# Performance work log

Measured on AMD Instinct MI355X. Metric: run time of the kernel, lower is better.

The kernel has to match this reference:

```python
import jax, jax.numpy as jnp
import numpy as np

N, E = 50000, 800000
IN, HID, H, OUT = 128, 32, 4, 32
NEG_SLOPE = 0.2


def _gatv2_layer(x, edge_index, Wl, bl, Wr, br, att, bias, heads, ch, concat):
    """One GATv2Conv layer (PyG semantics: add self-loops, lin_l on source,
    lin_r on target, e = att . leaky_relu(gl_src + gr_dst), segment softmax
    over incoming edges of each target, scatter-add weighted source messages)."""
    n = x.shape[0]
    loop = jnp.arange(n)
    src = jnp.concatenate([edge_index[0], loop])
    dst = jnp.concatenate([edge_index[1], loop])

    gl = (x @ Wl + bl).reshape(n, heads, ch)   # source transform [N,H,C]
    gr = (x @ Wr + br).reshape(n, heads, ch)   # target transform [N,H,C]

    m = jax.nn.leaky_relu(gl[src] + gr[dst], NEG_SLOPE)   # [E+N,H,C]
    e = jnp.einsum('ehc,hc->eh', m, att)                   # [E+N,H]

    # numerically stable segment softmax over dst
    emax = jax.lax.stop_gradient(jax.ops.segment_max(e, dst, num_segments=n))
    ex = jnp.exp(e - emax[dst])
    denom = jax.ops.segment_sum(ex, dst, num_segments=n)
    alpha = ex / denom[dst]                                # [E+N,H]

    out = jax.ops.segment_sum(alpha[:, :, None] * gl[src], dst, num_segments=n)  # [N,H,C]
    out = out.reshape(n, heads * ch) if concat else out.mean(axis=1)
    return out + bias


def setup_inputs() -> dict:
    key = jax.random.key(0)
    ks = jax.random.split(key, 16)
    s = 0.05
    return {
        'x': jax.random.normal(ks[0], (N, IN), dtype=jnp.float32),
        'edge_index': jax.random.randint(ks[1], (2, E), 0, N, dtype=jnp.int32),
        # layer 1: IN -> HID, H heads, concat
        'Wl1': jax.random.normal(ks[2], (IN, H * HID), dtype=jnp.float32) * s,
        'bl1': jnp.zeros((H * HID,), dtype=jnp.float32),
        'Wr1': jax.random.normal(ks[3], (IN, H * HID), dtype=jnp.float32) * s,
        'br1': jnp.zeros((H * HID,), dtype=jnp.float32),
        'att1': jax.random.normal(ks[4], (H, HID), dtype=jnp.float32) * s,
        'bias1': jnp.zeros((H * HID,), dtype=jnp.float32),
        # layer 2: H*HID -> OUT, 1 head, no concat
        'Wl2': jax.random.normal(ks[5], (H * HID, OUT), dtype=jnp.float32) * s,
        'bl2': jnp.zeros((OUT,), dtype=jnp.float32),
        'Wr2': jax.random.normal(ks[6], (H * HID, OUT), dtype=jnp.float32) * s,
        'br2': jnp.zeros((OUT,), dtype=jnp.float32),
        'att2': jax.random.normal(ks[7], (1, OUT), dtype=jnp.float32) * s,
        'bias2': jnp.zeros((OUT,), dtype=jnp.float32),
    }


def reference(x, edge_index, Wl1, bl1, Wr1, br1, att1, bias1,
              Wl2, bl2, Wr2, br2, att2, bias2):
    h = jax.nn.elu(_gatv2_layer(x, edge_index, Wl1, bl1, Wr1, br1, att1, bias1, H, HID, True))
    # dropout inactive in eval mode
    return _gatv2_layer(h, edge_index, Wl2, bl2, Wr2, br2, att2, bias2, 1, OUT, False)
```

## Files before the change

kernel.cpp:

```cpp
#include <hip/hip_runtime.h>

#define NNODES 50000
#define NEDGES 800000
#define ETOT   (NNODES + NEDGES)
#define NEG 0.2f
#define BKTS 196
#define P1E 4096
#define NP1 ((ETOT + P1E - 1) / P1E)
#define GEMM1_NB ((NNODES + 31) / 32)
#define GEMM1_H1 782
#define GEMM1_H2 (GEMM1_NB - GEMM1_H1)

typedef unsigned short ushort_t;
typedef unsigned int uint_t;
typedef __attribute__((ext_vector_type(8))) short short8;
typedef __attribute__((ext_vector_type(4))) float f32x4;

__device__ __forceinline__ ushort_t f2bf(float f) {
  uint_t u = __float_as_uint(f);
  u += 0x7FFFu + ((u >> 16) & 1u);
  return (ushort_t)(u >> 16);
}
__device__ __forceinline__ float bf2f(ushort_t h) {
  return __uint_as_float((uint_t)h << 16);
}


__device__ __forceinline__ void coarse_hist_body(int bid, int tid,
    const int* __restrict__ ei, int* __restrict__ pcnt, int* c ) {
  for (int i = tid; i < BKTS; i += 256) c[i] = 0;
  __syncthreads();
  int e0 = bid * P1E;
#pragma unroll
  for (int t = 0; t < P1E / 256; ++t) {
    int i = e0 + t * 256 + tid;
    if (i < ETOT) {
      int dst = (i < NEDGES) ? ei[NEDGES + i] : (i - NEDGES);
      atomicAdd(&c[dst >> 8], 1);
    }
  }
  __syncthreads();
  for (int i = tid; i < BKTS; i += 256)
    pcnt[i * NP1 + bid] = c[i];
}

__device__ __forceinline__ void prep_w_body(int k, int n,
    const float* __restrict__ Wl1, const float* __restrict__ Wr1,
    ushort_t* __restrict__ WtHi, ushort_t* __restrict__ WtLo) {
  float w = (n < 128) ? Wl1[k * 128 + n] : Wr1[k * 128 + (n - 128)];
  ushort_t h = f2bf(w);
  WtHi[n * 128 + k] = h;
  WtLo[n * 128 + k] = f2bf(w - bf2f(h));
}

__device__ __forceinline__ void bin1_body(int bid, int tid,
    const int* __restrict__ ei, const int* __restrict__ bucketStart,
    const int* __restrict__ goffArr, uint_t* __restrict__ binned, char* smemc) {
  int* cnt   = (int*)smemc;
  int* pref  = cnt + BKTS;
  int* fillL = pref + BKTS;
  uint_t* stage = (uint_t*)(fillL + BKTS);
  int e0 = bid * P1E;
  for (int i = tid; i < BKTS; i += 256) { cnt[i] = 0; fillL[i] = 0; }
  __syncthreads();
  uint_t mypk[P1E / 256];
#pragma unroll
  for (int t = 0; t < P1E / 256; ++t) {
    int i = e0 + t * 256 + tid;
    if (i < ETOT) {
      int dst = (i < NEDGES) ? ei[NEDGES + i] : (i - NEDGES);
      int src = (i < NEDGES) ? ei[i] : dst;
      int b = dst >> 8;
      mypk[t] = (uint_t)src | ((uint_t)(dst & 255) << 16) | ((uint_t)b << 24);
      atomicAdd(&cnt[b], 1);
    } else mypk[t] = 0xFFFFFFFFu;
  }
  __syncthreads();
  if (tid < 64) {
    int carry = 0;
    for (int k0 = 0; k0 < BKTS; k0 += 64) {
      int k = k0 + tid;
      int v = (k < BKTS) ? cnt[k] : 0;
      int s = v;
      for (int off = 1; off < 64; off <<= 1) {
        int u = __shfl_up(s, off);
        if (tid >= off) s += u;
      }
      if (k < BKTS) pref[k] = carry + s - v;
      carry += __shfl(s, 63);
    }
  }
  __syncthreads();
#pragma unroll
  for (int t = 0; t < P1E / 256; ++t) {
    uint_t pk = mypk[t];
    int b = pk >> 24;
    if (b < BKTS) {
      int p = pref[b] + atomicAdd(&fillL[b], 1);
      stage[p] = pk;
    }
  }
  __syncthreads();
  int total = (e0 + P1E <= ETOT) ? P1E : (ETOT - e0);
  for (int j = tid; j < total; j += 256) {
    uint_t pk = stage[j];
    int b = pk >> 24;
    binned[bucketStart[b] + goffArr[b * NP1 + bid] + (j - pref[b])] = pk;
  }
}

__device__ __forceinline__ void bin2_body(int b, int tid,
    const uint_t* __restrict__ binned, const int* __restrict__ bucketStart,
    int* __restrict__ rowptr, int* __restrict__ csrc, char* smemc) {
  int* cnt   = (int*)smemc;
  int* pref  = cnt + 256;
  int* fillL = pref + 256;
  int* outS  = fillL + 256;
  int base = bucketStart[b];
  int cntAll = bucketStart[b + 1] - base;
  cnt[tid] = 0; fillL[tid] = 0;
  __syncthreads();
  for (int j = tid; j < cntAll; j += 256)
    atomicAdd(&cnt[(binned[base + j] >> 16) & 255], 1);
  __syncthreads();
  if (tid < 64) {
    int carry = 0;
    for (int k0 = 0; k0 < 256; k0 += 64) {
      int k = k0 + tid;
      int v = cnt[k];
      int s = v;
      for (int off = 1; off < 64; off <<= 1) {
        int u = __shfl_up(s, off);
        if (tid >= off) s += u;
      }
      pref[k] = carry + s - v;
      carry += __shfl(s, 63);
    }
  }
  __syncthreads();
  int node = b * 256 + tid;
  if (node < NNODES) rowptr[node] = base + pref[tid];
  for (int j = tid; j < cntAll; j += 256) {
    uint_t pk = binned[base + j];
    int d = (pk >> 16) & 255;
    int p = pref[d] + atomicAdd(&fillL[d], 1);
    outS[p] = (int)(pk & 0xFFFF);
  }
  __syncthreads();
  for (int j = tid; j < cntAll; j += 256)
    csrc[base + j] = outS[j];
}

__device__ __forceinline__ void gemm1_body(int m0, int tid,
    const float* __restrict__ x,
    const ushort_t* __restrict__ WtHi, const ushort_t* __restrict__ WtLo,
    const float* __restrict__ bl1, const float* __restrict__ br1,
    ushort_t* __restrict__ gl1, ushort_t* __restrict__ gr1, char* smem) {
  constexpr int LDA = 132;
  ushort_t (*Ahi)[LDA] = (ushort_t(*)[LDA])smem;
  ushort_t (*Alo)[LDA] = (ushort_t(*)[LDA])(smem + 32 * LDA * 2);
  float (*Cs)[260] = (float(*)[260])smem;
#pragma unroll
  for (int i = 0; i < 4; ++i) {
    int it = i * 256 + tid;
    int row = it >> 5, c4 = it & 31;
    int gm = m0 + row;
    float4 v = (gm < NNODES) ? *(const float4*)&x[(size_t)gm * 128 + 4 * c4]
                             : make_float4(0.f, 0.f, 0.f, 0.f);
    ushort_t h0 = f2bf(v.x), h1 = f2bf(v.y), h2 = f2bf(v.z), h3 = f2bf(v.w);
    ushort_t l0 = f2bf(v.x - bf2f(h0)), l1 = f2bf(v.y - bf2f(h1));
    ushort_t l2 = f2bf(v.z - bf2f(h2)), l3 = f2bf(v.w - bf2f(h3));
    uint2 ph, pl;
    ph.x = (uint_t)h0 | ((uint_t)h1 << 16); ph.y = (uint_t)h2 | ((uint_t)h3 << 16);
    pl.x = (uint_t)l0 | ((uint_t)l1 << 16); pl.y = (uint_t)l2 | ((uint_t)l3 << 16);
    *(uint2*)&Ahi[row][4 * c4] = ph;
    *(uint2*)&Alo[row][4 * c4] = pl;
  }
  __syncthreads();
  int wave = tid >> 6, lane = tid & 63;
  int quad = lane >> 4, nl = lane & 15;
  int nb = wave * 64;
  f32x4 acc[2][4];
#pragma unroll
  for (int tm = 0; tm < 2; ++tm)
#pragma unroll
    for (int tn = 0; tn < 4; ++tn) acc[tm][tn] = (f32x4){0.f, 0.f, 0.f, 0.f};

#pragma unroll
  for (int kc = 0; kc < 4; ++kc) {
    int klane = kc * 32 + quad * 8;
    short8 ah[2], al[2], bh[4], bl[4];
#pragma unroll
    for (int tm = 0; tm < 2; ++tm) {
      ah[tm] = *(const short8*)&Ahi[16 * tm + nl][klane];
      al[tm] = *(const short8*)&Alo[16 * tm + nl][klane];
    }
#pragma unroll
    for (int tn = 0; tn < 4; ++tn) {
      size_t wo = (size_t)(nb + 16 * tn + nl) * 128 + klane;
      bh[tn] = *(const short8*)&WtHi[wo];
      bl[tn] = *(const short8*)&WtLo[wo];
    }
#pragma unroll
    for (int tm = 0; tm < 2; ++tm)
#pragma unroll
      for (int tn = 0; tn < 4; ++tn) {
        acc[tm][tn] = __builtin_amdgcn_mfma_f32_16x16x32_bf16(ah[tm], bh[tn], acc[tm][tn], 0, 0, 0);
        acc[tm][tn] = __builtin_amdgcn_mfma_f32_16x16x32_bf16(ah[tm], bl[tn], acc[tm][tn], 0, 0, 0);
        acc[tm][tn] = __builtin_amdgcn_mfma_f32_16x16x32_bf16(al[tm], bh[tn], acc[tm][tn], 0, 0, 0);
      }
  }
  float bb[4];
#pragma unroll
  for (int tn = 0; tn < 4; ++tn) {
    int n = nb + 16 * tn + nl;
    bb[tn] = (n < 128) ? bl1[n] : br1[n - 128];
  }
  __syncthreads();
#pragma unroll
  for (int tm = 0; tm < 2; ++tm)
#pragma unroll
    for (int tn = 0; tn < 4; ++tn)
#pragma unroll
      for (int r = 0; r < 4; ++r)
        Cs[16 * tm + 4 * quad + r][nb + 16 * tn + nl] = acc[tm][tn][r] + bb[tn];
  __syncthreads();
#pragma unroll
  for (int i = 0; i < 2; ++i) {
    int it = i * 256 + tid;
    int row = it >> 4, oc = (it & 15) * 8;
    int gm = m0 + row;
    if (gm < NNODES) {
      uint4 pk;
      pk.x = (uint_t)f2bf(Cs[row][oc + 0]) | ((uint_t)f2bf(Cs[row][oc + 1]) << 16);
      pk.y = (uint_t)f2bf(Cs[row][oc + 2]) | ((uint_t)f2bf(Cs[row][oc + 3]) << 16);
      pk.z = (uint_t)f2bf(Cs[row][oc + 4]) | ((uint_t)f2bf(Cs[row][oc + 5]) << 16);
      pk.w = (uint_t)f2bf(Cs[row][oc + 6]) | ((uint_t)f2bf(Cs[row][oc + 7]) << 16);
      *(uint4*)&gl1[(size_t)gm * 128 + oc] = pk;
    }
  }
#pragma unroll
  for (int i = 0; i < 2; ++i) {
    int it = i * 256 + tid;
    int row = it >> 4, oc = (it & 15) * 8;
    int gm = m0 + row;
    if (gm < NNODES) {
      uint4 pk;
      pk.x = (uint_t)f2bf(Cs[row][128 + oc + 0]) | ((uint_t)f2bf(Cs[row][128 + oc + 1]) << 16);
      pk.y = (uint_t)f2bf(Cs[row][128 + oc + 2]) | ((uint_t)f2bf(Cs[row][128 + oc + 3]) << 16);
      pk.z = (uint_t)f2bf(Cs[row][128 + oc + 4]) | ((uint_t)f2bf(Cs[row][128 + oc + 5]) << 16);
      pk.w = (uint_t)f2bf(Cs[row][128 + oc + 6]) | ((uint_t)f2bf(Cs[row][128 + oc + 7]) << 16);
      *(uint4*)&gr1[(size_t)gm * 128 + oc] = pk;
    }
  }
}


__global__ __launch_bounds__(256) void fusedA(const int* __restrict__ ei,
    int* __restrict__ pcnt,
    const float* __restrict__ Wl1, const float* __restrict__ Wr1,
    ushort_t* __restrict__ WtHi, ushort_t* __restrict__ WtLo) {
  __shared__ int c[BKTS];
  int bid = blockIdx.x, tid = threadIdx.x;
  if (bid < NP1) coarse_hist_body(bid, tid, ei, pcnt, c);
  else           prep_w_body(bid - NP1, tid, Wl1, Wr1, WtHi, WtLo);
}

__global__ __launch_bounds__(64) void coarse_scan(const int* __restrict__ pcnt,
                                                  int* __restrict__ goffArr,
                                                  int* __restrict__ tot) {
  int b = blockIdx.x;
  int lane = threadIdx.x;
  int carry = 0;
  for (int k0 = 0; k0 < NP1; k0 += 64) {
    int k = k0 + lane;
    int v = (k < NP1) ? pcnt[b * NP1 + k] : 0;
    int s = v;
    for (int off = 1; off < 64; off <<= 1) {
      int u = __shfl_up(s, off);
      if (lane >= off) s += u;
    }
    if (k < NP1) goffArr[b * NP1 + k] = carry + s - v;
    carry += __shfl(s, 63);
  }
  if (lane == 0) tot[b] = carry;
}

__global__ __launch_bounds__(64) void bucket_scan(const int* __restrict__ tot,
                                                  int* __restrict__ bucketStart,
                                                  int* __restrict__ rowptr) {
  int lane = threadIdx.x;
  int carry = 0;
  for (int k0 = 0; k0 < BKTS; k0 += 64) {
    int k = k0 + lane;
    int v = (k < BKTS) ? tot[k] : 0;
    int s = v;
    for (int off = 1; off < 64; off <<= 1) {
      int u = __shfl_up(s, off);
      if (lane >= off) s += u;
    }
    if (k < BKTS) bucketStart[k] = carry + s - v;
    carry += __shfl(s, 63);
  }
  if (lane == 0) {
    bucketStart[BKTS] = carry;
    rowptr[NNODES] = ETOT;
  }
}

__global__ __launch_bounds__(256) void fusedB(const int* __restrict__ ei,
    const int* __restrict__ bucketStart, const int* __restrict__ goffArr,
    uint_t* __restrict__ binned,
    const float* __restrict__ x,
    const ushort_t* __restrict__ WtHi, const ushort_t* __restrict__ WtLo,
    const float* __restrict__ bl1, const float* __restrict__ br1,
    ushort_t* __restrict__ gl1, ushort_t* __restrict__ gr1) {
  __shared__ __align__(16) char smem[32 * 260 * 4];
  int bid = blockIdx.x, tid = threadIdx.x;
  if (bid < NP1) bin1_body(bid, tid, ei, bucketStart, goffArr, binned, smem);
  else gemm1_body((bid - NP1) * 32, tid, x, WtHi, WtLo, bl1, br1, gl1, gr1, smem);
}

__global__ __launch_bounds__(256) void fusedC(const uint_t* __restrict__ binned,
    const int* __restrict__ bucketStart, int* __restrict__ rowptr,
    int* __restrict__ csrc,
    const float* __restrict__ x,
    const ushort_t* __restrict__ WtHi, const ushort_t* __restrict__ WtLo,
    const float* __restrict__ bl1, const float* __restrict__ br1,
    ushort_t* __restrict__ gl1, ushort_t* __restrict__ gr1) {
  __shared__ __align__(16) char smem[32 * 260 * 4];
  int bid = blockIdx.x, tid = threadIdx.x;
  if (bid < BKTS) bin2_body(bid, tid, binned, bucketStart, rowptr, csrc, smem);
  else gemm1_body((GEMM1_H1 + bid - BKTS) * 32, tid, x, WtHi, WtLo, bl1, br1, gl1, gr1, smem);
}

__global__ __launch_bounds__(128) void gemm2_tile(
    const ushort_t* __restrict__ A,
    const float* __restrict__ W1, const float* __restrict__ b1,
    const float* __restrict__ W2, const float* __restrict__ b2,
    ushort_t* __restrict__ G1, ushort_t* __restrict__ G2) {
  constexpr int K = 128, KC = 32, BM = 128, BN = 64, MCOLS = 32, NT = 128;
  constexpr int LDA = BM + 4;
  __shared__ float AsT[KC][LDA];
  __shared__ float Ws[KC][BN];
  int row0 = blockIdx.x * BM;
  int tid = threadIdx.x;
  int tx = tid % (BN / 8), ty = tid / (BN / 8);
  float acc[8][8];
#pragma unroll
  for (int i = 0; i < 8; ++i)
#pragma unroll
    for (int j = 0; j < 8; ++j) acc[i][j] = 0.f;

  for (int kc = 0; kc < K; kc += KC) {
#pragma unroll
    for (int item = tid; item < BM * (KC / 4); item += NT) {
      int r = item >> 3, f4 = item & 7;
      int grow = row0 + r;
      uint2 u = (grow < NNODES)
          ? *(const uint2*)&A[(size_t)grow * K + kc + 4 * f4]
          : make_uint2(0u, 0u);
      AsT[4 * f4 + 0][r] = __uint_as_float(u.x << 16);
      AsT[4 * f4 + 1][r] = __uint_as_float(u.x & 0xffff0000u);
      AsT[4 * f4 + 2][r] = __uint_as_float(u.y << 16);
      AsT[4 * f4 + 3][r] = __uint_as_float(u.y & 0xffff0000u);
    }
#pragma unroll
    for (int item = tid; item < KC * (BN / 4); item += NT) {
      int k = item / (BN / 4), c4 = item % (BN / 4);
      int ccat = 4 * c4;
      const float* src = (ccat < MCOLS)
          ? &W1[(size_t)(kc + k) * MCOLS + ccat]
          : &W2[(size_t)(kc + k) * MCOLS + ccat - MCOLS];
      *(float4*)&Ws[k][4 * c4] = *(const float4*)src;
    }
    __syncthreads();
#pragma unroll 8
    for (int k = 0; k < KC; ++k) {
      float4 a0 = *(const float4*)&AsT[k][4 * ty];
      float4 a1 = *(const float4*)&AsT[k][BM / 2 + 4 * ty];
      float4 w0 = *(const float4*)&Ws[k][4 * tx];
      float4 w1 = *(const float4*)&Ws[k][BN / 2 + 4 * tx];
      float av[8] = {a0.x, a0.y, a0.z, a0.w, a1.x, a1.y, a1.z, a1.w};
      float wv[8] = {w0.x, w0.y, w0.z, w0.w, w1.x, w1.y, w1.z, w1.w};
#pragma unroll
      for (int i = 0; i < 8; ++i)
#pragma unroll
        for (int j = 0; j < 8; ++j) acc[i][j] = fmaf(av[i], wv[j], acc[i][j]);
    }
    __syncthreads();
  }
#pragma unroll
  for (int i = 0; i < 8; ++i) {
    int row = row0 + (i < 4 ? 4 * ty + i : BM / 2 + 4 * ty + (i - 4));
    if (row >= NNODES) continue;
#pragma unroll
    for (int jj = 0; jj < 2; ++jj) {
      int ccat = (jj == 0 ? 4 * tx : BN / 2 + 4 * tx);
      float o0 = acc[i][4 * jj + 0], o1 = acc[i][4 * jj + 1];
      float o2 = acc[i][4 * jj + 2], o3 = acc[i][4 * jj + 3];
      if (ccat < MCOLS) {
        float4 bb = *(const float4*)&b1[ccat];
        uint2 pk;
        pk.x = (uint_t)f2bf(o0 + bb.x) | ((uint_t)f2bf(o1 + bb.y) << 16);
        pk.y = (uint_t)f2bf(o2 + bb.z) | ((uint_t)f2bf(o3 + bb.w) << 16);
        *(uint2*)&G1[(size_t)row * MCOLS + ccat] = pk;
      } else {
        int c = ccat - MCOLS;
        float4 bb = *(const float4*)&b2[c];
        uint2 pk;
        pk.x = (uint_t)f2bf(o0 + bb.x) | ((uint_t)f2bf(o1 + bb.y) << 16);
        pk.y = (uint_t)f2bf(o2 + bb.z) | ((uint_t)f2bf(o3 + bb.w) << 16);
        *(uint2*)&G2[(size_t)row * MCOLS + c] = pk;
      }
    }
  }
}

__global__ __launch_bounds__(128) void gat1_edge(const int* __restrict__ rowptr,
                          const int* __restrict__ csrc,
                          const ushort_t* __restrict__ glb,
                          const ushort_t* __restrict__ grb,
                          const float* __restrict__ att, const float* __restrict__ bias,
                          ushort_t* __restrict__ hout) {
  int node = blockIdx.x * 2 + (threadIdx.x >> 6);
  if (node >= NNODES) return;
  int lane = threadIdx.x & 63;
  int eslot = lane >> 4;
  int q = lane & 15;
  int c8 = q * 8;
  const float C6 = 0.8656170245333781f;
  const float C4 = 0.5770780163555854f;
  float4 av0 = *(const float4*)(att + c8);
  float4 av1 = *(const float4*)(att + c8 + 4);
  float4 a60, a61, a40, a41;
  a60.x = C6 * av0.x; a60.y = C6 * av0.y; a60.z = C6 * av0.z; a60.w = C6 * av0.w;
  a61.x = C6 * av1.x; a61.y = C6 * av1.y; a61.z = C6 * av1.z; a61.w = C6 * av1.w;
  a40.x = C4 * av0.x; a40.y = C4 * av0.y; a40.z = C4 * av0.z; a40.w = C4 * av0.w;
  a41.x = C4 * av1.x; a41.y = C4 * av1.y; a41.z = C4 * av1.z; a41.w = C4 * av1.w;
  uint4 ug = *(const uint4*)(grb + (size_t)node * 128 + c8);
  float4 gr0, gr1v;
  gr0.x = __uint_as_float(ug.x << 16);  gr0.y = __uint_as_float(ug.x & 0xffff0000u);
  gr0.z = __uint_as_float(ug.y << 16);  gr0.w = __uint_as_float(ug.y & 0xffff0000u);
  gr1v.x = __uint_as_float(ug.z << 16); gr1v.y = __uint_as_float(ug.z & 0xffff0000u);
  gr1v.z = __uint_as_float(ug.w << 16); gr1v.w = __uint_as_float(ug.w & 0xffff0000u);
  int start = rowptr[node], end = rowptr[node + 1];
  float denom = 0.f;
  float4 A0 = make_float4(0.f, 0.f, 0.f, 0.f);
  float4 A1 = make_float4(0.f, 0.f, 0.f, 0.f);
  const char* glc = (const char*)glb;
  uint_t coff = (uint_t)(c8 * 2);
  for (int b = start; b < end; b += 64) {
    int nb = end - b; if (nb > 64) nb = 64;
    int sidx = (lane < nb) ? csrc[b + lane] : 0;
    bool pv0 = eslot < nb;
    int s0 = __shfl(sidx, eslot);
    uint4 up0 = *(const uint4*)(glc + (((uint_t)s0 << 8) + coff));
    int j1 = 4 + eslot;
    bool pv1 = j1 < nb;
    int s1 = __shfl(sidx, pv1 ? j1 : 0);
    uint4 up1 = *(const uint4*)(glc + (((uint_t)s1 << 8) + coff));
    for (int j = 0; j < nb; j += 4) {
      int jn = j + 8 + eslot;
      bool pvn = jn < nb;
      int sn = __shfl(sidx, pvn ? jn : 0);
      uint4 upn = *(const uint4*)(glc + (((uint_t)sn << 8) + coff));
      float4 g0, g1;
      g0.x = __uint_as_float(up0.x << 16);
      g0.y = __uint_as_float(up0.x & 0xffff0000u);
      g0.z = __uint_as_float(up0.y << 16);
      g0.w = __uint_as_float(up0.y & 0xffff0000u);
      g1.x = __uint_as_float(up0.z << 16);
      g1.y = __uint_as_float(up0.z & 0xffff0000u);
      g1.z = __uint_as_float(up0.w << 16);
      g1.w = __uint_as_float(up0.w & 0xffff0000u);
      float t, v;
      t = g0.x + gr0.x;  v = fmaf(a40.x, fabsf(t), a60.x * t);
      t = g0.y + gr0.y;  v = fmaf(a60.y, t, v); v = fmaf(a40.y, fabsf(t), v);
      t = g0.z + gr0.z;  v = fmaf(a60.z, t, v); v = fmaf(a40.z, fabsf(t), v);
      t = g0.w + gr0.w;  v = fmaf(a60.w, t, v); v = fmaf(a40.w, fabsf(t), v);
      t = g1.x + gr1v.x; v = fmaf(a61.x, t, v); v = fmaf(a41.x, fabsf(t), v);
      t = g1.y + gr1v.y; v = fmaf(a61.y, t, v); v = fmaf(a41.y, fabsf(t), v);
      t = g1.z + gr1v.z; v = fmaf(a61.z, t, v); v = fmaf(a41.z, fabsf(t), v);
      t = g1.w + gr1v.w; v = fmaf(a61.w, t, v); v = fmaf(a41.w, fabsf(t), v);
      v += __shfl_xor(v, 1); v += __shfl_xor(v, 2);
      float ex = pv0 ? exp2f(v) : 0.f;
      denom += ex;
      A0.x = fmaf(ex, g0.x, A0.x); A0.y = fmaf(ex, g0.y, A0.y);
      A0.z = fmaf(ex, g0.z, A0.z); A0.w = fmaf(ex, g0.w, A0.w);
      A1.x = fmaf(ex, g1.x, A1.x); A1.y = fmaf(ex, g1.y, A1.y);
      A1.z = fmaf(ex, g1.z, A1.z); A1.w = fmaf(ex, g1.w, A1.w);
      up0 = up1; pv0 = pv1;
      up1 = upn; pv1 = pvn;
    }
  }
  denom += __shfl_xor(denom, 16); denom += __shfl_xor(denom, 32);
  A0.x += __shfl_xor(A0.x, 16); A0.x += __shfl_xor(A0.x, 32);
  A0.y += __shfl_xor(A0.y, 16); A0.y += __shfl_xor(A0.y, 32);
  A0.z += __shfl_xor(A0.z, 16); A0.z += __shfl_xor(A0.z, 32);
  A0.w += __shfl_xor(A0.w, 16); A0.w += __shfl_xor(A0.w, 32);
  A1.x += __shfl_xor(A1.x, 16); A1.x += __shfl_xor(A1.x, 32);
  A1.y += __shfl_xor(A1.y, 16); A1.y += __shfl_xor(A1.y, 32);
  A1.z += __shfl_xor(A1.z, 16); A1.z += __shfl_xor(A1.z, 32);
  A1.w += __shfl_xor(A1.w, 16); A1.w += __shfl_xor(A1.w, 32);
  if (eslot < 2) {
    float inv = __builtin_amdgcn_rcpf(denom);
    float4 Ax;
    Ax.x = (eslot == 0) ? A0.x : A1.x;
    Ax.y = (eslot == 0) ? A0.y : A1.y;
    Ax.z = (eslot == 0) ? A0.z : A1.z;
    Ax.w = (eslot == 0) ? A0.w : A1.w;
    int off = c8 + 4 * eslot;
    float4 bv = *(const float4*)(bias + off);
    float o0 = Ax.x * inv + bv.x, o1 = Ax.y * inv + bv.y;
    float o2 = Ax.z * inv + bv.z, o3 = Ax.w * inv + bv.w;
    o0 = o0 > 0.f ? o0 : __expf(o0) - 1.f;
    o1 = o1 > 0.f ? o1 : __expf(o1) - 1.f;
    o2 = o2 > 0.f ? o2 : __expf(o2) - 1.f;
    o3 = o3 > 0.f ? o3 : __expf(o3) - 1.f;
    uint2 pk;
    pk.x = (uint_t)f2bf(o0) | ((uint_t)f2bf(o1) << 16);
    pk.y = (uint_t)f2bf(o2) | ((uint_t)f2bf(o3) << 16);
    *(uint2*)&hout[(size_t)node * 128 + off] = pk;
  }
}

__global__ __launch_bounds__(128) void gat2_edge(const int* __restrict__ rowptr,
                          const int* __restrict__ csrc,
                          const ushort_t* __restrict__ gl, const ushort_t* __restrict__ gr,
                          const float* __restrict__ att, const float* __restrict__ bias,
                          float* __restrict__ out) {
  int node = blockIdx.x * 2 + (threadIdx.x >> 6);
  if (node >= NNODES) return;
  int lane = threadIdx.x & 63;
  int eslot = lane >> 3;
  int q = lane & 7;
  int c4 = q * 4;
  const float C6 = 0.8656170245333781f;
  const float C4f = 0.5770780163555854f;
  float4 avc = *(const float4*)(att + c4);
  float4 a6, a4;
  a6.x = C6 * avc.x; a6.y = C6 * avc.y; a6.z = C6 * avc.z; a6.w = C6 * avc.w;
  a4.x = C4f * avc.x; a4.y = C4f * avc.y; a4.z = C4f * avc.z; a4.w = C4f * avc.w;
  uint2 ugr = *(const uint2*)(gr + (size_t)node * 32 + c4);
  float4 grd;
  grd.x = __uint_as_float(ugr.x << 16); grd.y = __uint_as_float(ugr.x & 0xffff0000u);
  grd.z = __uint_as_float(ugr.y << 16); grd.w = __uint_as_float(ugr.y & 0xffff0000u);
  int start = rowptr[node], end = rowptr[node + 1];
  float denom = 0.f;
  float4 A = make_float4(0.f, 0.f, 0.f, 0.f);
  const char* glc = (const char*)gl;
  uint_t coff = (uint_t)(c4 * 2);
  for (int b = start; b < end; b += 64) {
    int nb = end - b; if (nb > 64) nb = 64;
    int sidx = (lane < nb) ? csrc[b + lane] : 0;
    bool pv0 = eslot < nb;
    int s0 = __shfl(sidx, eslot);
    uint2 u0 = *(const uint2*)(glc + (((uint_t)s0 << 6) + coff));
    int j1 = 8 + eslot;
    bool pv1 = j1 < nb;
    int s1 = __shfl(sidx, pv1 ? j1 : 0);
    uint2 u1 = *(const uint2*)(glc + (((uint_t)s1 << 6) + coff));
    for (int j = 0; j < nb; j += 8) {
      int jn = j + 16 + eslot;
      bool pvn = jn < nb;
      int sn = __shfl(sidx, pvn ? jn : 0);
      uint2 un = *(const uint2*)(glc + (((uint_t)sn << 6) + coff));
      float4 g;
      g.x = __uint_as_float(u0.x << 16); g.y = __uint_as_float(u0.x & 0xffff0000u);
      g.z = __uint_as_float(u0.y << 16); g.w = __uint_as_float(u0.y & 0xffff0000u);
      float t, v;
      t = g.x + grd.x; v = fmaf(a4.x, fabsf(t), a6.x * t);
      t = g.y + grd.y; v = fmaf(a6.y, t, v); v = fmaf(a4.y, fabsf(t), v);
      t = g.z + grd.z; v = fmaf(a6.z, t, v); v = fmaf(a4.z, fabsf(t), v);
      t = g.w + grd.w; v = fmaf(a6.w, t, v); v = fmaf(a4.w, fabsf(t), v);
      v += __shfl_xor(v, 1); v += __shfl_xor(v, 2); v += __shfl_xor(v, 4);
      float ex = pv0 ? exp2f(v) : 0.f;
      denom += ex;
      A.x = fmaf(ex, g.x, A.x); A.y = fmaf(ex, g.y, A.y);
      A.z = fmaf(ex, g.z, A.z); A.w = fmaf(ex, g.w, A.w);
      u0 = u1; pv0 = pv1;
      u1 = un; pv1 = pvn;
    }
  }
  denom += __shfl_xor(denom, 8); denom += __shfl_xor(denom, 16); denom += __shfl_xor(denom, 32);
  A.x += __shfl_xor(A.x, 8); A.x += __shfl_xor(A.x, 16); A.x += __shfl_xor(A.x, 32);
  A.y += __shfl_xor(A.y, 8); A.y += __shfl_xor(A.y, 16); A.y += __shfl_xor(A.y, 32);
  A.z += __shfl_xor(A.z, 8); A.z += __shfl_xor(A.z, 16); A.z += __shfl_xor(A.z, 32);
  A.w += __shfl_xor(A.w, 8); A.w += __shfl_xor(A.w, 16); A.w += __shfl_xor(A.w, 32);
  if (eslot == 0) {
    float inv = __builtin_amdgcn_rcpf(denom);
    float4 bv = *(const float4*)(bias + c4);
    float4 o;
    o.x = A.x * inv + bv.x; o.y = A.y * inv + bv.y;
    o.z = A.z * inv + bv.z; o.w = A.w * inv + bv.w;
    *(float4*)(out + (size_t)node * 32 + c4) = o;
  }
}

extern "C" void kernel_launch(void* const* d_in, const int* in_sizes, int n_in,
                              void* d_out, int out_size, void* d_ws, size_t ws_size,
                              hipStream_t stream) {
  const float* x     = (const float*)d_in[0];
  const int*   ei    = (const int*)  d_in[1];
  const float* Wl1   = (const float*)d_in[2];
  const float* bl1   = (const float*)d_in[3];
  const float* Wr1   = (const float*)d_in[4];
  const float* br1   = (const float*)d_in[5];
  const float* att1  = (const float*)d_in[6];
  const float* bias1 = (const float*)d_in[7];
  const float* Wl2   = (const float*)d_in[8];
  const float* bl2   = (const float*)d_in[9];
  const float* Wr2   = (const float*)d_in[10];
  const float* br2   = (const float*)d_in[11];
  const float* att2  = (const float*)d_in[12];
  const float* bias2 = (const float*)d_in[13];
  float* out = (float*)d_out;

  char* w = (char*)d_ws;
  auto carve = [&](size_t bytes) {
    char* p = w;
    w += (bytes + 255) & ~(size_t)255;
    return p;
  };
  ushort_t* gl1 = (ushort_t*)carve((size_t)NNODES * 128 * 2);
  ushort_t* gr1 = (ushort_t*)carve((size_t)NNODES * 128 * 2);
  ushort_t* h   = (ushort_t*)carve((size_t)NNODES * 128 * 2);
  ushort_t* gl2 = (ushort_t*)carve((size_t)NNODES * 32 * 2);
  ushort_t* gr2 = (ushort_t*)carve((size_t)NNODES * 32 * 2);
  ushort_t* WtHi = (ushort_t*)carve((size_t)256 * 128 * 2);
  ushort_t* WtLo = (ushort_t*)carve((size_t)256 * 128 * 2);
  int* pcnt    = (int*)carve((size_t)NP1 * BKTS * 4);
  int* goffArr = (int*)carve((size_t)NP1 * BKTS * 4);
  int* tot     = (int*)carve((size_t)BKTS * 4);
  int* bucketStart = (int*)carve((size_t)(BKTS + 1) * 4);
  int* rowptr = (int*)carve((size_t)(NNODES + 1) * 4);
  uint_t* binned = (uint_t*)carve((size_t)ETOT * 4);
  int* csrc = (int*)carve((size_t)ETOT * 4);

  fusedA<<<NP1 + 128, 256, 0, stream>>>(ei, pcnt, Wl1, Wr1, WtHi, WtLo);
  coarse_scan<<<BKTS, 64, 0, stream>>>(pcnt, goffArr, tot);
  bucket_scan<<<1, 64, 0, stream>>>(tot, bucketStart, rowptr);
  fusedB<<<NP1 + GEMM1_H1, 256, 0, stream>>>(ei, bucketStart, goffArr, binned,
                                             x, WtHi, WtLo, bl1, br1, gl1, gr1);
  fusedC<<<BKTS + GEMM1_H2, 256, 0, stream>>>(binned, bucketStart, rowptr, csrc,
                                              x, WtHi, WtLo, bl1, br1, gl1, gr1);
  gat1_edge<<<(NNODES + 1) / 2, 128, 0, stream>>>(rowptr, csrc, gl1, gr1, att1, bias1, h);
  gemm2_tile<<<(NNODES + 127) / 128, 128, 0, stream>>>(h, Wl2, bl2, Wr2, br2, gl2, gr2);
  gat2_edge<<<(NNODES + 1) / 2, 128, 0, stream>>>(rowptr, csrc, gl2, gr2, att2, bias2, out);
}
```

Measured before the change: 243.6 us.

## Fold bucket scan into coarse scan via last-block atomic, shrink GEMM staging smem

Removes the separate single-block bucket_scan launch. The last coarse_scan block, detected with an atomic counter that fusedA resets, performs the bucket prefix scan instead. The GEMM1 epilogue now stages the output tile through shared memory in two 16-row halves, which shrinks the shared-memory arrays in fusedB and fusedC and should allow more blocks to be resident. It also moves more GEMM1 tiles into fusedB (split changed from 782 to 1000). The costs are extra barriers in the epilogue and reliance on threadfence/atomic ordering for correctness.

```diff
diff --git a/kernel.cpp b/kernel.cpp
--- a/kernel.cpp
+++ b/kernel.cpp
@@ -8,7 +8,7 @@
 #define P1E 4096
 #define NP1 ((ETOT + P1E - 1) / P1E)
 #define GEMM1_NB ((NNODES + 31) / 32)
-#define GEMM1_H1 782
+#define GEMM1_H1 1000
 #define GEMM1_H2 (GEMM1_NB - GEMM1_H1)
 
 typedef unsigned short ushort_t;
@@ -218,40 +218,32 @@
   }
   __syncthreads();
 #pragma unroll
-  for (int tm = 0; tm < 2; ++tm)
+  for (int half = 0; half < 2; ++half) {
 #pragma unroll
     for (int tn = 0; tn < 4; ++tn)
 #pragma unroll
       for (int r = 0; r < 4; ++r)
-        Cs[16 * tm + 4 * quad + r][nb + 16 * tn + nl] = acc[tm][tn][r] + bb[tn];
-  __syncthreads();
-#pragma unroll
-  for (int i = 0; i < 2; ++i) {
-    int it = i * 256 + tid;
-    int row = it >> 4, oc = (it & 15) * 8;
-    int gm = m0 + row;
-    if (gm < NNODES) {
-      uint4 pk;
-      pk.x = (uint_t)f2bf(Cs[row][oc + 0]) | ((uint_t)f2bf(Cs[row][oc + 1]) << 16);
-      pk.y = (uint_t)f2bf(Cs[row][oc + 2]) | ((uint_t)f2bf(Cs[row][oc + 3]) << 16);
-      pk.z = (uint_t)f2bf(Cs[row][oc + 4]) | ((uint_t)f2bf(Cs[row][oc + 5]) << 16);
-      pk.w = (uint_t)f2bf(Cs[row][oc + 6]) | ((uint_t)f2bf(Cs[row][oc + 7]) << 16);
-      *(uint4*)&gl1[(size_t)gm * 128 + oc] = pk;
-    }
-  }
-#pragma unroll
-  for (int i = 0; i < 2; ++i) {
-    int it = i * 256 + tid;
-    int row = it >> 4, oc = (it & 15) * 8;
-    int gm = m0 + row;
-    if (gm < NNODES) {
-      uint4 pk;
-      pk.x = (uint_t)f2bf(Cs[row][128 + oc + 0]) | ((uint_t)f2bf(Cs[row][128 + oc + 1]) << 16);
-      pk.y = (uint_t)f2bf(Cs[row][128 + oc + 2]) | ((uint_t)f2bf(Cs[row][128 + oc + 3]) << 16);
-      pk.z = (uint_t)f2bf(Cs[row][128 + oc + 4]) | ((uint_t)f2bf(Cs[row][128 + oc + 5]) << 16);
-      pk.w = (uint_t)f2bf(Cs[row][128 + oc + 6]) | ((uint_t)f2bf(Cs[row][128 + oc + 7]) << 16);
-      *(uint4*)&gr1[(size_t)gm * 128 + oc] = pk;
-    }
+        Cs[4 * quad + r][nb + 16 * tn + nl] = acc[half][tn][r] + bb[tn];
+    __syncthreads();
+    {
+      int row = tid >> 4, oc = (tid & 15) * 8;
+      int gm = m0 + half * 16 + row;
+      if (gm < NNODES) {
+        uint4 pk;
+        pk.x = (uint_t)f2bf(Cs[row][oc + 0]) | ((uint_t)f2bf(Cs[row][oc + 1]) << 16);
+        pk.y = (uint_t)f2bf(Cs[row][oc + 2]) | ((uint_t)f2bf(Cs[row][oc + 3]) << 16);
+        pk.z = (uint_t)f2bf(Cs[row][oc + 4]) | ((uint_t)f2bf(Cs[row][oc + 5]) << 16);
+        pk.w = (uint_t)f2bf(Cs[row][oc + 6]) | ((uint_t)f2bf(Cs[row][oc + 7]) << 16);
+        *(uint4*)&gl1[(size_t)gm * 128 + oc] = pk;
+        uint4 pk2;
+        pk2.x = (uint_t)f2bf(Cs[row][128 + oc + 0]) | ((uint_t)f2bf(Cs[row][128 + oc + 1]) << 16);
+        pk2.y = (uint_t)f2bf(Cs[row][128 + oc + 2]) | ((uint_t)f2bf(Cs[row][128 + oc + 3]) << 16);
+        pk2.z = (uint_t)f2bf(Cs[row][128 + oc + 4]) | ((uint_t)f2bf(Cs[row][128 + oc + 5]) << 16);
+        pk2.w = (uint_t)f2bf(Cs[row][128 + oc + 6]) | ((uint_t)f2bf(Cs[row][128 + oc + 7]) << 16);
+        *(uint4*)&gr1[(size_t)gm * 128 + oc] = pk2;
+      }
+    }
+    __syncthreads();
   }
 }
 
@@ -259,16 +251,21 @@
 __global__ __launch_bounds__(256) void fusedA(const int* __restrict__ ei,
     int* __restrict__ pcnt,
     const float* __restrict__ Wl1, const float* __restrict__ Wr1,
-    ushort_t* __restrict__ WtHi, ushort_t* __restrict__ WtLo) {
+    ushort_t* __restrict__ WtHi, ushort_t* __restrict__ WtLo,
+    int* __restrict__ done) {
   __shared__ int c[BKTS];
   int bid = blockIdx.x, tid = threadIdx.x;
+  if (bid == NP1 && tid == 0) *done = 0;
   if (bid < NP1) coarse_hist_body(bid, tid, ei, pcnt, c);
   else           prep_w_body(bid - NP1, tid, Wl1, Wr1, WtHi, WtLo);
 }
 
 __global__ __launch_bounds__(64) void coarse_scan(const int* __restrict__ pcnt,
                                                   int* __restrict__ goffArr,
-                                                  int* __restrict__ tot) {
+                                                  int* __restrict__ tot,
+                                                  int* __restrict__ bucketStart,
+                                                  int* __restrict__ rowptr,
+                                                  int* __restrict__ done) {
   int b = blockIdx.x;
   int lane = threadIdx.x;
   int carry = 0;
@@ -284,27 +281,28 @@
     carry += __shfl(s, 63);
   }
   if (lane == 0) tot[b] = carry;
-}
-
-__global__ __launch_bounds__(64) void bucket_scan(const int* __restrict__ tot,
-                                                  int* __restrict__ bucketStart,
-                                                  int* __restrict__ rowptr) {
-  int lane = threadIdx.x;
-  int carry = 0;
-  for (int k0 = 0; k0 < BKTS; k0 += 64) {
-    int k = k0 + lane;
-    int v = (k < BKTS) ? tot[k] : 0;
-    int s = v;
-    for (int off = 1; off < 64; off <<= 1) {
-      int u = __shfl_up(s, off);
-      if (lane >= off) s += u;
-    }
-    if (k < BKTS) bucketStart[k] = carry + s - v;
-    carry += __shfl(s, 63);
-  }
-  if (lane == 0) {
-    bucketStart[BKTS] = carry;
-    rowptr[NNODES] = ETOT;
+  __threadfence();
+  int old = 0;
+  if (lane == 0) old = atomicAdd(done, 1);
+  old = __shfl(old, 0);
+  if (old == BKTS - 1) {
+    __threadfence();
+    int carry2 = 0;
+    for (int k0 = 0; k0 < BKTS; k0 += 64) {
+      int k = k0 + lane;
+      int v = (k < BKTS) ? tot[k] : 0;
+      int s = v;
+      for (int off = 1; off < 64; off <<= 1) {
+        int u = __shfl_up(s, off);
+        if (lane >= off) s += u;
+      }
+      if (k < BKTS) bucketStart[k] = carry2 + s - v;
+      carry2 += __shfl(s, 63);
+    }
+    if (lane == 0) {
+      bucketStart[BKTS] = carry2;
+      rowptr[NNODES] = ETOT;
+    }
   }
 }
 
@@ -315,7 +313,7 @@
     const ushort_t* __restrict__ WtHi, const ushort_t* __restrict__ WtLo,
     const float* __restrict__ bl1, const float* __restrict__ br1,
     ushort_t* __restrict__ gl1, ushort_t* __restrict__ gr1) {
-  __shared__ __align__(16) char smem[32 * 260 * 4];
+  __shared__ __align__(16) char smem[18736];
   int bid = blockIdx.x, tid = threadIdx.x;
   if (bid < NP1) bin1_body(bid, tid, ei, bucketStart, goffArr, binned, smem);
   else gemm1_body((bid - NP1) * 32, tid, x, WtHi, WtLo, bl1, br1, gl1, gr1, smem);
@@ -328,7 +326,7 @@
     const ushort_t* __restrict__ WtHi, const ushort_t* __restrict__ WtLo,
     const float* __restrict__ bl1, const float* __restrict__ br1,
     ushort_t* __restrict__ gl1, ushort_t* __restrict__ gr1) {
-  __shared__ __align__(16) char smem[32 * 260 * 4];
+  __shared__ __align__(16) char smem[27648];
   int bid = blockIdx.x, tid = threadIdx.x;
   if (bid < BKTS) bin2_body(bid, tid, binned, bucketStart, rowptr, csrc, smem);
   else gemm1_body((GEMM1_H1 + bid - BKTS) * 32, tid, x, WtHi, WtLo, bl1, br1, gl1, gr1, smem);
@@ -637,10 +635,10 @@
   int* rowptr = (int*)carve((size_t)(NNODES + 1) * 4);
   uint_t* binned = (uint_t*)carve((size_t)ETOT * 4);
   int* csrc = (int*)carve((size_t)ETOT * 4);
-
-  fusedA<<<NP1 + 128, 256, 0, stream>>>(ei, pcnt, Wl1, Wr1, WtHi, WtLo);
-  coarse_scan<<<BKTS, 64, 0, stream>>>(pcnt, goffArr, tot);
-  bucket_scan<<<1, 64, 0, stream>>>(tot, bucketStart, rowptr);
+  int* done = (int*)carve(4);
+
+  fusedA<<<NP1 + 128, 256, 0, stream>>>(ei, pcnt, Wl1, Wr1, WtHi, WtLo, done);
+  coarse_scan<<<BKTS, 64, 0, stream>>>(pcnt, goffArr, tot, bucketStart, rowptr, done);
   fusedB<<<NP1 + GEMM1_H1, 256, 0, stream>>>(ei, bucketStart, goffArr, binned,
                                              x, WtHi, WtLo, bl1, br1, gl1, gr1);
   fusedC<<<BKTS + GEMM1_H2, 256, 0, stream>>>(binned, bucketStart, rowptr, csrc,
```

New measurement: 247.0 us. About the same (+1.4%).
